# Performance work log

Measured on AMD Instinct MI355X. Metric: run time of the kernel, lower is better.

## Reference

```python
import jax, jax.numpy as jnp
import numpy as np

W_LEN, BSZ, EMBED, NHEADS = 1024, 16, 512, 8
HEAD_DIM = EMBED // NHEADS
LN_EPS = 1e-5


def setup_inputs() -> dict:
    key = jax.random.key(0)
    ks = jax.random.split(key, 7)
    s = 1.0 / np.sqrt(EMBED)
    return {
        "feat": jax.random.normal(ks[0], (W_LEN, BSZ, EMBED), dtype=jnp.float32),
        "in_proj_w": jax.random.normal(ks[1], (3 * EMBED, EMBED), dtype=jnp.float32) * s,
        "in_proj_b": jax.random.normal(ks[2], (3 * EMBED,), dtype=jnp.float32) * 0.02,
        "out_w": jax.random.normal(ks[3], (EMBED, EMBED), dtype=jnp.float32) * s,
        "out_b": jax.random.normal(ks[4], (EMBED,), dtype=jnp.float32) * 0.02,
        "ln_g": jnp.ones((EMBED,), dtype=jnp.float32),
        "ln_b": jnp.zeros((EMBED,), dtype=jnp.float32),
    }


def _layernorm(x, g, b):
    mu = jnp.mean(x, axis=-1, keepdims=True)
    var = jnp.mean(jnp.square(x - mu), axis=-1, keepdims=True)
    return (x - mu) * jax.lax.rsqrt(var + LN_EPS) * g + b


def reference(feat, in_proj_w, in_proj_b, out_w, out_b, ln_g, ln_b):
    w, bsz, embed = feat.shape
    x = _layernorm(feat, ln_g, ln_b)
    # fused qkv projection (self-attention branch of the torch code)
    qkv = x @ in_proj_w.T + in_proj_b                      # [w, b, 3E]
    q, k, v = jnp.split(qkv, 3, axis=-1)
    scaling = float(HEAD_DIM) ** -0.5
    q = (q * scaling).reshape(w, bsz, NHEADS, HEAD_DIM)
    k = k.reshape(w, bsz, NHEADS, HEAD_DIM)
    v = v.reshape(w, bsz, NHEADS, HEAD_DIM)
    # scores [b, h, w, w2]
    attn = jnp.einsum('wnhd,vnhd->nhwv', q, k)
    attn = jax.nn.softmax(attn, axis=-1)
    v_out = jnp.einsum('nhwv,vnhd->wnhd', attn, v).reshape(w, bsz, embed)
    v_out = v_out @ out_w.T + out_b
    return feat + v_out
```

## Files before the change

### kernel.cpp

```cpp
#include <hip/hip_runtime.h>
#include <math.h>

#define W_LEN 1024
#define BSZ 16
#define EMBED 512
#define NHEADS 8
#define HEAD_DIM 64
#define TOKENS (W_LEN * BSZ)
#define LN_EPS 1e-5f

typedef __bf16 bf16_t;
typedef bf16_t bf16x8 __attribute__((ext_vector_type(8)));
typedef float f32x4 __attribute__((ext_vector_type(4)));

__device__ inline unsigned short f2bf(float f) {
    unsigned int u = __float_as_uint(f);
    u += 0x7fffu + ((u >> 16) & 1u);
    return (unsigned short)(u >> 16);
}

__device__ __forceinline__ void async16(const void* g, void* l) {
    __builtin_amdgcn_global_load_lds(
        (__attribute__((address_space(1))) void*)g,
        (__attribute__((address_space(3))) void*)l, 16, 0, 0);
}

__global__ __launch_bounds__(256) void cvt_f32_bf16(const float* __restrict__ src,
                                                    unsigned short* __restrict__ dst) {
    int i = (blockIdx.x * 256 + threadIdx.x) * 4;
    float4 f = *(const float4*)(src + i);
    uint2 p;
    p.x = (unsigned)f2bf(f.x) | ((unsigned)f2bf(f.y) << 16);
    p.y = (unsigned)f2bf(f.z) | ((unsigned)f2bf(f.w) << 16);
    *(uint2*)(dst + i) = p;
}

__global__ __launch_bounds__(256) void ln_kernel(
    const float* __restrict__ feat, const float* __restrict__ g,
    const float* __restrict__ b, unsigned short* __restrict__ xln)
{
    int tid   = threadIdx.x;
    int token = blockIdx.x * 4 + (tid >> 6);
    int lane  = tid & 63;
    const float* row = feat + (size_t)token * EMBED;

    float x[8];
    *(float4*)(x)     = *(const float4*)(row + lane * 4);
    *(float4*)(x + 4) = *(const float4*)(row + 256 + lane * 4);

    float sum = 0.f, ssq = 0.f;
#pragma unroll
    for (int i = 0; i < 8; i++) { sum += x[i]; ssq += x[i] * x[i]; }
#pragma unroll
    for (int off = 32; off > 0; off >>= 1) {
        sum += __shfl_xor(sum, off, 64);
        ssq += __shfl_xor(ssq, off, 64);
    }
    float mu  = sum * (1.0f / EMBED);
    float var = ssq * (1.0f / EMBED) - mu * mu;
    float rs  = rsqrtf(var + LN_EPS);

    float gg[8], bb[8], o[8];
    *(float4*)(gg)     = *(const float4*)(g + lane * 4);
    *(float4*)(gg + 4) = *(const float4*)(g + 256 + lane * 4);
    *(float4*)(bb)     = *(const float4*)(b + lane * 4);
    *(float4*)(bb + 4) = *(const float4*)(b + 256 + lane * 4);
#pragma unroll
    for (int i = 0; i < 8; i++) o[i] = (x[i] - mu) * rs * gg[i] + bb[i];

    unsigned short* orow = xln + (size_t)token * EMBED;
    uint2 lo, hi;
    lo.x = (unsigned)f2bf(o[0]) | ((unsigned)f2bf(o[1]) << 16);
    lo.y = (unsigned)f2bf(o[2]) | ((unsigned)f2bf(o[3]) << 16);
    hi.x = (unsigned)f2bf(o[4]) | ((unsigned)f2bf(o[5]) << 16);
    hi.y = (unsigned)f2bf(o[6]) | ((unsigned)f2bf(o[7]) << 16);
    *(uint2*)(orow + lane * 4)       = lo;
    *(uint2*)(orow + 256 + lane * 4) = hi;
}

__device__ __forceinline__ void gemm_core(const unsigned short* __restrict__ A,
                                          const unsigned short* __restrict__ Bt,
                                          int i0, int j0,
                                          unsigned short (*As0)[32], unsigned short (*As1)[32],
                                          unsigned short (*Bs0)[32], unsigned short (*Bs1)[32],
                                          f32x4 acc[4][4])
{
    int t = threadIdx.x;
    int wave = t >> 6, lane = t & 63, quad = lane >> 4, l16 = lane & 15;
    int wm = (wave >> 1) * 64, wn = (wave & 1) * 64;
    int srow = t >> 2, scol = (t & 3) * 8;
    const unsigned short* ga0 = A  + (size_t)(i0 + srow) * EMBED + scol;
    const unsigned short* ga1 = A  + (size_t)(i0 + srow + 64) * EMBED + scol;
    const unsigned short* gb0 = Bt + (size_t)(j0 + srow) * EMBED + scol;
    const unsigned short* gb1 = Bt + (size_t)(j0 + srow + 64) * EMBED + scol;

    for (int k0 = 0; k0 < EMBED; k0 += 64) {
        __syncthreads();
        async16(ga0 + k0,      &As0[srow][scol]);
        async16(ga1 + k0,      &As0[srow + 64][scol]);
        async16(gb0 + k0,      &Bs0[srow][scol]);
        async16(gb1 + k0,      &Bs0[srow + 64][scol]);
        async16(ga0 + k0 + 32, &As1[srow][scol]);
        async16(ga1 + k0 + 32, &As1[srow + 64][scol]);
        async16(gb0 + k0 + 32, &Bs1[srow][scol]);
        async16(gb1 + k0 + 32, &Bs1[srow + 64][scol]);
        __syncthreads();

#pragma unroll
        for (int h = 0; h < 2; h++) {
            unsigned short (*Ah)[32] = h ? As1 : As0;
            unsigned short (*Bh)[32] = h ? Bs1 : Bs0;
            bf16x8 af[4], bfr[4];
#pragma unroll
            for (int m = 0; m < 4; m++) af[m]  = *(const bf16x8*)&Ah[wm + m * 16 + l16][quad * 8];
#pragma unroll
            for (int n = 0; n < 4; n++) bfr[n] = *(const bf16x8*)&Bh[wn + n * 16 + l16][quad * 8];
#pragma unroll
            for (int m = 0; m < 4; m++)
#pragma unroll
                for (int n = 0; n < 4; n++)
                    acc[m][n] = __builtin_amdgcn_mfma_f32_16x16x32_bf16(af[m], bfr[n], acc[m][n], 0, 0, 0);
        }
    }
}

__global__ __launch_bounds__(256) void qkv_gemm_mfma(
    const unsigned short* __restrict__ A, const unsigned short* __restrict__ Bt,
    const float* __restrict__ bias, unsigned short* __restrict__ qo,
    unsigned short* __restrict__ ko, unsigned short* __restrict__ vo)
{
    __shared__ unsigned short As0[128][32], As1[128][32];
    __shared__ unsigned short Bs0[128][32], Bs1[128][32];
    f32x4 acc[4][4];
    const f32x4 z = {0.f, 0.f, 0.f, 0.f};
#pragma unroll
    for (int m = 0; m < 4; m++)
#pragma unroll
        for (int n = 0; n < 4; n++) acc[m][n] = z;

    int i0 = blockIdx.x * 128, j0 = blockIdx.y * 128;
    gemm_core(A, Bt, i0, j0, As0, As1, Bs0, Bs1, acc);

    int t = threadIdx.x, wave = t >> 6, lane = t & 63, quad = lane >> 4, l16 = lane & 15;
    int wm = (wave >> 1) * 64, wn = (wave & 1) * 64;
    int seg = j0 >> 9;
    unsigned short* outp = (seg == 0) ? qo : ((seg == 1) ? ko : vo);
    float scale = (seg == 0) ? 0.125f : 1.0f;

    float bj[4]; int hh[4], dd[4];
#pragma unroll
    for (int n = 0; n < 4; n++) {
        int j = j0 + wn + n * 16 + l16;
        bj[n] = bias[j];
        hh[n] = (j >> 6) & 7;
        dd[n] = j & 63;
    }
#pragma unroll
    for (int m = 0; m < 4; m++)
#pragma unroll
        for (int r = 0; r < 4; r++) {
            int token = i0 + wm + m * 16 + quad * 4 + r;
            int w  = token >> 4;
            int b_ = token & 15;
#pragma unroll
            for (int n = 0; n < 4; n++) {
                float val = (acc[m][n][r] + bj[n]) * scale;
                size_t idx;
                if (seg == 2)
                    idx = ((size_t)(b_ * NHEADS + hh[n]) * HEAD_DIM + dd[n]) * W_LEN + w;
                else
                    idx = (((size_t)(b_ * NHEADS + hh[n]) * W_LEN + w) << 6) + dd[n];
                outp[idx] = f2bf(val);
            }
        }
}

__global__ __launch_bounds__(256) void out_gemm_mfma(
    const unsigned short* __restrict__ A, const unsigned short* __restrict__ Bt,
    const float* __restrict__ bias, const float* __restrict__ feat,
    float* __restrict__ out)
{
    __shared__ unsigned short As0[128][32], As1[128][32];
    __shared__ unsigned short Bs0[128][32], Bs1[128][32];
    f32x4 acc[4][4];
    const f32x4 z = {0.f, 0.f, 0.f, 0.f};
#pragma unroll
    for (int m = 0; m < 4; m++)
#pragma unroll
        for (int n = 0; n < 4; n++) acc[m][n] = z;

    int i0 = blockIdx.x * 128, j0 = blockIdx.y * 128;
    gemm_core(A, Bt, i0, j0, As0, As1, Bs0, Bs1, acc);

    int t = threadIdx.x, wave = t >> 6, lane = t & 63, quad = lane >> 4, l16 = lane & 15;
    int wm = (wave >> 1) * 64, wn = (wave & 1) * 64;

    float bj[4];
#pragma unroll
    for (int n = 0; n < 4; n++) bj[n] = bias[j0 + wn + n * 16 + l16];
#pragma unroll
    for (int m = 0; m < 4; m++)
#pragma unroll
        for (int r = 0; r < 4; r++) {
            int token = i0 + wm + m * 16 + quad * 4 + r;
#pragma unroll
            for (int n = 0; n < 4; n++) {
                int col = j0 + wn + n * 16 + l16;
                size_t idx = (size_t)token * EMBED + col;
                out[idx] = acc[m][n][r] + bj[n] + feat[idx];
            }
        }
}

__global__ __launch_bounds__(256, 4) void attn_mfma(
    const unsigned short* __restrict__ q, const unsigned short* __restrict__ k,
    const unsigned short* __restrict__ vT, unsigned short* __restrict__ outp)
{
    __shared__ union {
        unsigned short Q[128][72];
        struct {
            unsigned short K[64][64];
            unsigned short V[64][64];
            unsigned short P[4][32][72];
        } s;
    } sm;

    int t = threadIdx.x, wave = t >> 6, lane = t & 63, quad = lane >> 4, l16 = lane & 15;
    int bh = blockIdx.x;
    int q0 = blockIdx.y * 128;
    const unsigned short* qp  = q  + ((size_t)bh * W_LEN + q0) * HEAD_DIM;
    const unsigned short* kp  = k  + (size_t)bh * W_LEN * HEAD_DIM;
    const unsigned short* vtp = vT + (size_t)bh * HEAD_DIM * W_LEN;

    {
        int qr = t >> 1, qc0 = (t & 1) * 32;
#pragma unroll
        for (int c = 0; c < 32; c += 8)
            *(uint4*)&sm.Q[qr][qc0 + c] = *(const uint4*)(qp + (size_t)qr * 64 + qc0 + c);
    }
    __syncthreads();
    bf16x8 qf[2][2];
#pragma unroll
    for (int nt = 0; nt < 2; nt++)
#pragma unroll
        for (int ks = 0; ks < 2; ks++)
            qf[nt][ks] = *(const bf16x8*)&sm.Q[wave * 32 + nt * 16 + l16][ks * 32 + quad * 8];
    __syncthreads();

    float l_st[2] = {0.f, 0.f};
    f32x4 o_acc[4][2];
    const f32x4 z = {0.f, 0.f, 0.f, 0.f};
#pragma unroll
    for (int m = 0; m < 4; m++)
#pragma unroll
        for (int n = 0; n < 2; n++) o_acc[m][n] = z;

    unsigned short* kl = &sm.s.K[0][0];
    unsigned short* vl = &sm.s.V[0][0];
    int sr = t >> 3;
    int sc = ((t & 7) ^ (sr & 7)) * 8;

    for (int kt = 0; kt < W_LEN; kt += 64) {
        __syncthreads();
#pragma unroll
        for (int j = 0; j < 2; j++) {
            int r = sr + j * 32;
            async16(kp  + (size_t)(kt + r) * 64 + sc, kl + (size_t)(t + j * 256) * 8);
            async16(vtp + (size_t)r * W_LEN + kt + sc, vl + (size_t)(t + j * 256) * 8);
        }
        __syncthreads();

        f32x4 s[4][2];
#pragma unroll
        for (int mt = 0; mt < 4; mt++)
#pragma unroll
            for (int nt = 0; nt < 2; nt++) s[mt][nt] = z;
#pragma unroll
        for (int ks = 0; ks < 2; ks++) {
            int swz = (((ks * 4 + quad) ^ (l16 & 7)) * 8);
            bf16x8 kf[4];
#pragma unroll
            for (int mt = 0; mt < 4; mt++)
                kf[mt] = *(const bf16x8*)(kl + (size_t)(mt * 16 + l16) * 64 + swz);
#pragma unroll
            for (int mt = 0; mt < 4; mt++)
#pragma unroll
                for (int nt = 0; nt < 2; nt++)
                    s[mt][nt] = __builtin_amdgcn_mfma_f32_16x16x32_bf16(kf[mt], qf[nt][ks], s[mt][nt], 0, 0, 0);
        }

#pragma unroll
        for (int nt = 0; nt < 2; nt++) {
            float sum = 0.f;
#pragma unroll
            for (int mt = 0; mt < 4; mt++)
#pragma unroll
                for (int r = 0; r < 4; r++) {
                    float p = __expf(s[mt][nt][r]);
                    s[mt][nt][r] = p;
                    sum += p;
                }
            sum += __shfl_xor(sum, 16, 64);
            sum += __shfl_xor(sum, 32, 64);
            l_st[nt] += sum;
        }

#pragma unroll
        for (int nt = 0; nt < 2; nt++)
#pragma unroll
            for (int mt = 0; mt < 4; mt++) {
                uint2 pk;
                pk.x = (unsigned)f2bf(s[mt][nt][0]) | ((unsigned)f2bf(s[mt][nt][1]) << 16);
                pk.y = (unsigned)f2bf(s[mt][nt][2]) | ((unsigned)f2bf(s[mt][nt][3]) << 16);
                *(uint2*)&sm.s.P[wave][nt * 16 + l16][mt * 16 + quad * 4] = pk;
            }
        asm volatile("s_waitcnt lgkmcnt(0)" ::: "memory");

#pragma unroll
        for (int ks = 0; ks < 2; ks++) {
            int swz = (((ks * 4 + quad) ^ (l16 & 7)) * 8);
            bf16x8 vf[4], pf[2];
#pragma unroll
            for (int mtd = 0; mtd < 4; mtd++)
                vf[mtd] = *(const bf16x8*)(vl + (size_t)(mtd * 16 + l16) * 64 + swz);
#pragma unroll
            for (int nt = 0; nt < 2; nt++)
                pf[nt] = *(const bf16x8*)&sm.s.P[wave][nt * 16 + l16][ks * 32 + quad * 8];
#pragma unroll
            for (int mtd = 0; mtd < 4; mtd++)
#pragma unroll
                for (int nt = 0; nt < 2; nt++)
                    o_acc[mtd][nt] = __builtin_amdgcn_mfma_f32_16x16x32_bf16(vf[mtd], pf[nt], o_acc[mtd][nt], 0, 0, 0);
        }
    }

    int b_ = bh >> 3, h = bh & 7;
#pragma unroll
    for (int nt = 0; nt < 2; nt++) {
        int w = q0 + wave * 32 + nt * 16 + l16;
        int token = w * BSZ + b_;
        float inv = 1.0f / l_st[nt];
#pragma unroll
        for (int mtd = 0; mtd < 4; mtd++) {
            uint2 pk;
            pk.x = (unsigned)f2bf(o_acc[mtd][nt][0] * inv) |
                   ((unsigned)f2bf(o_acc[mtd][nt][1] * inv) << 16);
            pk.y = (unsigned)f2bf(o_acc[mtd][nt][2] * inv) |
                   ((unsigned)f2bf(o_acc[mtd][nt][3] * inv) << 16);
            *(uint2*)(outp + (size_t)token * EMBED + h * HEAD_DIM + mtd * 16 + quad * 4) = pk;
        }
    }
}

extern "C" void kernel_launch(void* const* d_in, const int* in_sizes, int n_in,
                              void* d_out, int out_size, void* d_ws, size_t ws_size,
                              hipStream_t stream) {
    const float* feat  = (const float*)d_in[0];
    const float* in_w  = (const float*)d_in[1];
    const float* in_b  = (const float*)d_in[2];
    const float* out_w = (const float*)d_in[3];
    const float* out_b = (const float*)d_in[4];
    const float* ln_g  = (const float*)d_in[5];
    const float* ln_b  = (const float*)d_in[6];
    float* out = (float*)d_out;

    char* ws = (char*)d_ws;
    const size_t SZB = (size_t)TOKENS * EMBED * sizeof(unsigned short);
    unsigned short* xln = (unsigned short*)ws;
    unsigned short* qb  = (unsigned short*)(ws + SZB);
    unsigned short* kb  = (unsigned short*)(ws + 2 * SZB);
    unsigned short* vtb = (unsigned short*)(ws + 3 * SZB);
    unsigned short* ao  = (unsigned short*)(ws + 4 * SZB);
    unsigned short* wib = (unsigned short*)(ws + 5 * SZB);
    unsigned short* wob = (unsigned short*)(ws + 5 * SZB +
                                            (size_t)3 * EMBED * EMBED * sizeof(unsigned short));

    cvt_f32_bf16<<<(3 * EMBED * EMBED) / 1024, 256, 0, stream>>>(in_w, wib);
    cvt_f32_bf16<<<(EMBED * EMBED) / 1024, 256, 0, stream>>>(out_w, wob);
    ln_kernel<<<TOKENS / 4, 256, 0, stream>>>(feat, ln_g, ln_b, xln);
    qkv_gemm_mfma<<<dim3(TOKENS / 128, (3 * EMBED) / 128), 256, 0, stream>>>(
        xln, wib, in_b, qb, kb, vtb);
    attn_mfma<<<dim3(BSZ * NHEADS, W_LEN / 128), 256, 0, stream>>>(qb, kb, vtb, ao);
    out_gemm_mfma<<<dim3(TOKENS / 128, EMBED / 128), 256, 0, stream>>>(
        ao, wob, out_b, feat, out);
}
```

Baseline: 261.9 us.

## Register-prefetch next K/V tile in attention; vectorize V-transpose stores in QKV epilogue

The attention loop now loads the next K/V tile from global memory into registers while the current tile is being computed, then writes those registers to LDS at the top of the next iteration. This replaces direct async global-to-LDS loads that the kernel waited on before any compute. Separately, the QKV GEMM epilogue for the V segment packs four consecutive w positions into one 8-byte store instead of scattering 2-byte stores. The prefetch costs extra registers, which may lower occupancy, and on the last iteration it reloads the same tile redundantly.

Result: faster. 251.9 us (-3.8%).

```diff
diff --git a/kernel.cpp b/kernel.cpp
--- a/kernel.cpp
+++ b/kernel.cpp
@@ -144,8 +144,6 @@
     int t = threadIdx.x, wave = t >> 6, lane = t & 63, quad = lane >> 4, l16 = lane & 15;
     int wm = (wave >> 1) * 64, wn = (wave & 1) * 64;
     int seg = j0 >> 9;
-    unsigned short* outp = (seg == 0) ? qo : ((seg == 1) ? ko : vo);
-    float scale = (seg == 0) ? 0.125f : 1.0f;
 
     float bj[4]; int hh[4], dd[4];
 #pragma unroll
@@ -155,24 +153,39 @@
         hh[n] = (j >> 6) & 7;
         dd[n] = j & 63;
     }
-#pragma unroll
-    for (int m = 0; m < 4; m++)
-#pragma unroll
-        for (int r = 0; r < 4; r++) {
-            int token = i0 + wm + m * 16 + quad * 4 + r;
-            int w  = token >> 4;
-            int b_ = token & 15;
-#pragma unroll
-            for (int n = 0; n < 4; n++) {
-                float val = (acc[m][n][r] + bj[n]) * scale;
-                size_t idx;
-                if (seg == 2)
-                    idx = ((size_t)(b_ * NHEADS + hh[n]) * HEAD_DIM + dd[n]) * W_LEN + w;
-                else
-                    idx = (((size_t)(b_ * NHEADS + hh[n]) * W_LEN + w) << 6) + dd[n];
-                outp[idx] = f2bf(val);
+
+    if (seg == 2) {
+        int w0 = (i0 >> 4) + (wm >> 4);
+#pragma unroll
+        for (int n = 0; n < 4; n++)
+#pragma unroll
+            for (int r = 0; r < 4; r++) {
+                int b_ = quad * 4 + r;
+                uint2 pk;
+                pk.x = (unsigned)f2bf(acc[0][n][r] + bj[n]) |
+                       ((unsigned)f2bf(acc[1][n][r] + bj[n]) << 16);
+                pk.y = (unsigned)f2bf(acc[2][n][r] + bj[n]) |
+                       ((unsigned)f2bf(acc[3][n][r] + bj[n]) << 16);
+                size_t idx = ((size_t)((b_ * NHEADS + hh[n]) * HEAD_DIM + dd[n])) * W_LEN + w0;
+                *(uint2*)(vo + idx) = pk;
             }
-        }
+    } else {
+        unsigned short* outp = (seg == 0) ? qo : ko;
+        float scale = (seg == 0) ? 0.125f : 1.0f;
+#pragma unroll
+        for (int m = 0; m < 4; m++)
+#pragma unroll
+            for (int r = 0; r < 4; r++) {
+                int token = i0 + wm + m * 16 + quad * 4 + r;
+                int w  = token >> 4;
+                int b_ = token & 15;
+#pragma unroll
+                for (int n = 0; n < 4; n++) {
+                    size_t idx = (((size_t)(b_ * NHEADS + hh[n]) * W_LEN + w) << 6) + dd[n];
+                    outp[idx] = f2bf((acc[m][n][r] + bj[n]) * scale);
+                }
+            }
+    }
 }
 
 __global__ __launch_bounds__(256) void out_gemm_mfma(
@@ -260,15 +273,30 @@
     int sr = t >> 3;
     int sc = ((t & 7) ^ (sr & 7)) * 8;
 
+    uint4 kg[2], vg[2];
+#pragma unroll
+    for (int j = 0; j < 2; j++) {
+        int r = sr + j * 32;
+        kg[j] = *(const uint4*)(kp  + (size_t)r * 64 + sc);
+        vg[j] = *(const uint4*)(vtp + (size_t)r * W_LEN + sc);
+    }
+
     for (int kt = 0; kt < W_LEN; kt += 64) {
         __syncthreads();
 #pragma unroll
         for (int j = 0; j < 2; j++) {
+            *(uint4*)(kl + (size_t)(t + j * 256) * 8) = kg[j];
+            *(uint4*)(vl + (size_t)(t + j * 256) * 8) = vg[j];
+        }
+        __syncthreads();
+
+        int ktn = (kt + 64 < W_LEN) ? kt + 64 : kt;
+#pragma unroll
+        for (int j = 0; j < 2; j++) {
             int r = sr + j * 32;
-            async16(kp  + (size_t)(kt + r) * 64 + sc, kl + (size_t)(t + j * 256) * 8);
-            async16(vtp + (size_t)r * W_LEN + kt + sc, vl + (size_t)(t + j * 256) * 8);
-        }
-        __syncthreads();
+            kg[j] = *(const uint4*)(kp  + (size_t)(ktn + r) * 64 + sc);
+            vg[j] = *(const uint4*)(vtp + (size_t)r * W_LEN + ktn + sc);
+        }
 
         f32x4 s[4][2];
 #pragma unroll
```

## Store V untransposed and transpose in attention via register-prefetched LDS staging

Applied to the files above, without the earlier changes.

The QKV GEMM now writes V in the same [b,h,w,d] layout as Q and K, removing the strided transposed scatter in its epilogue. The attention kernel drops the async global-to-LDS loads and instead prefetches the next K/V tile into registers while the current tile is computed. K is copied to LDS as before, and V is transposed on the fly by packing pairs of rows into 32-bit LDS stores into a padded buffer. This targets the uncoalesced V-transpose writes in the GEMM and overlaps global load latency with compute, at the cost of more registers (risking occupancy at launch_bounds 256,4) and more LDS store instructions with possible bank conflicts.

New measurement: 218.5 us. 1.2x faster.

```diff
diff --git a/kernel.cpp b/kernel.cpp
--- a/kernel.cpp
+++ b/kernel.cpp
@@ -164,13 +164,8 @@
             int b_ = token & 15;
 #pragma unroll
             for (int n = 0; n < 4; n++) {
-                float val = (acc[m][n][r] + bj[n]) * scale;
-                size_t idx;
-                if (seg == 2)
-                    idx = ((size_t)(b_ * NHEADS + hh[n]) * HEAD_DIM + dd[n]) * W_LEN + w;
-                else
-                    idx = (((size_t)(b_ * NHEADS + hh[n]) * W_LEN + w) << 6) + dd[n];
-                outp[idx] = f2bf(val);
+                size_t idx = (((size_t)(b_ * NHEADS + hh[n]) * W_LEN + w) << 6) + dd[n];
+                outp[idx] = f2bf((acc[m][n][r] + bj[n]) * scale);
             }
         }
 }
@@ -214,13 +209,13 @@
 
 __global__ __launch_bounds__(256, 4) void attn_mfma(
     const unsigned short* __restrict__ q, const unsigned short* __restrict__ k,
-    const unsigned short* __restrict__ vT, unsigned short* __restrict__ outp)
+    const unsigned short* __restrict__ v, unsigned short* __restrict__ outp)
 {
     __shared__ union {
         unsigned short Q[128][72];
         struct {
             unsigned short K[64][64];
-            unsigned short V[64][64];
+            unsigned short V[64][72];
             unsigned short P[4][32][72];
         } s;
     } sm;
@@ -228,9 +223,9 @@
     int t = threadIdx.x, wave = t >> 6, lane = t & 63, quad = lane >> 4, l16 = lane & 15;
     int bh = blockIdx.x;
     int q0 = blockIdx.y * 128;
-    const unsigned short* qp  = q  + ((size_t)bh * W_LEN + q0) * HEAD_DIM;
-    const unsigned short* kp  = k  + (size_t)bh * W_LEN * HEAD_DIM;
-    const unsigned short* vtp = vT + (size_t)bh * HEAD_DIM * W_LEN;
+    const unsigned short* qp = q + ((size_t)bh * W_LEN + q0) * HEAD_DIM;
+    const unsigned short* kp = k + (size_t)bh * W_LEN * HEAD_DIM;
+    const unsigned short* vp = v + (size_t)bh * W_LEN * HEAD_DIM;
 
     {
         int qr = t >> 1, qc0 = (t & 1) * 32;
@@ -256,19 +251,36 @@
         for (int n = 0; n < 2; n++) o_acc[m][n] = z;
 
     unsigned short* kl = &sm.s.K[0][0];
-    unsigned short* vl = &sm.s.V[0][0];
     int sr = t >> 3;
     int sc = ((t & 7) ^ (sr & 7)) * 8;
+    int j2 = t & 31, vc = (t >> 5) * 8;
+
+    uint4 kg[2];
+    union { uint4 u; unsigned short sv[8]; } vg0, vg1;
+#pragma unroll
+    for (int j = 0; j < 2; j++)
+        kg[j] = *(const uint4*)(kp + (size_t)(sr + j * 32) * 64 + sc);
+    vg0.u = *(const uint4*)(vp + (size_t)(2 * j2) * 64 + vc);
+    vg1.u = *(const uint4*)(vp + (size_t)(2 * j2 + 1) * 64 + vc);
 
     for (int kt = 0; kt < W_LEN; kt += 64) {
         __syncthreads();
 #pragma unroll
-        for (int j = 0; j < 2; j++) {
-            int r = sr + j * 32;
-            async16(kp  + (size_t)(kt + r) * 64 + sc, kl + (size_t)(t + j * 256) * 8);
-            async16(vtp + (size_t)r * W_LEN + kt + sc, vl + (size_t)(t + j * 256) * 8);
+        for (int j = 0; j < 2; j++)
+            *(uint4*)(kl + (size_t)(t + j * 256) * 8) = kg[j];
+#pragma unroll
+        for (int i = 0; i < 8; i++) {
+            unsigned int pk = (unsigned)vg0.sv[i] | ((unsigned)vg1.sv[i] << 16);
+            *(unsigned int*)&sm.s.V[vc + i][2 * j2] = pk;
         }
         __syncthreads();
+
+        int ktn = (kt + 64 < W_LEN) ? kt + 64 : kt;
+#pragma unroll
+        for (int j = 0; j < 2; j++)
+            kg[j] = *(const uint4*)(kp + (size_t)(ktn + sr + j * 32) * 64 + sc);
+        vg0.u = *(const uint4*)(vp + (size_t)(ktn + 2 * j2) * 64 + vc);
+        vg1.u = *(const uint4*)(vp + (size_t)(ktn + 2 * j2 + 1) * 64 + vc);
 
         f32x4 s[4][2];
 #pragma unroll
@@ -318,11 +330,10 @@
 
 #pragma unroll
         for (int ks = 0; ks < 2; ks++) {
-            int swz = (((ks * 4 + quad) ^ (l16 & 7)) * 8);
             bf16x8 vf[4], pf[2];
 #pragma unroll
             for (int mtd = 0; mtd < 4; mtd++)
-                vf[mtd] = *(const bf16x8*)(vl + (size_t)(mtd * 16 + l16) * 64 + swz);
+                vf[mtd] = *(const bf16x8*)&sm.s.V[mtd * 16 + l16][ks * 32 + quad * 8];
 #pragma unroll
             for (int nt = 0; nt < 2; nt++)
                 pf[nt] = *(const bf16x8*)&sm.s.P[wave][nt * 16 + l16][ks * 32 + quad * 8];
@@ -369,7 +380,7 @@
     unsigned short* xln = (unsigned short*)ws;
     unsigned short* qb  = (unsigned short*)(ws + SZB);
     unsigned short* kb  = (unsigned short*)(ws + 2 * SZB);
-    unsigned short* vtb = (unsigned short*)(ws + 3 * SZB);
+    unsigned short* vb  = (unsigned short*)(ws + 3 * SZB);
     unsigned short* ao  = (unsigned short*)(ws + 4 * SZB);
     unsigned short* wib = (unsigned short*)(ws + 5 * SZB);
     unsigned short* wob = (unsigned short*)(ws + 5 * SZB +
@@ -379,8 +390,8 @@
     cvt_f32_bf16<<<(EMBED * EMBED) / 1024, 256, 0, stream>>>(out_w, wob);
     ln_kernel<<<TOKENS / 4, 256, 0, stream>>>(feat, ln_g, ln_b, xln);
     qkv_gemm_mfma<<<dim3(TOKENS / 128, (3 * EMBED) / 128), 256, 0, stream>>>(
-        xln, wib, in_b, qb, kb, vtb);
-    attn_mfma<<<dim3(BSZ * NHEADS, W_LEN / 128), 256, 0, stream>>>(qb, kb, vtb, ao);
+        xln, wib, in_b, qb, kb, vb);
+    attn_mfma<<<dim3(BSZ * NHEADS, W_LEN / 128), 256, 0, stream>>>(qb, kb, vb, ao);
     out_gemm_mfma<<<dim3(TOKENS / 128, EMBED / 128), 256, 0, stream>>>(
         ao, wob, out_b, feat, out);
 }
```
